# Optimization experiments

Measured on AMD Instinct MI355X. Metric: run time of the kernel, lower is better.

## Reference

```python
import jax, jax.numpy as jnp
import numpy as np

INPUT_DIM = 512
HIDDEN_DIM = 512


def setup_inputs() -> dict:
    key = jax.random.key(0)
    k1, k2 = jax.random.split(key, 2)
    T, B = 2048, 32
    x = jax.random.normal(k1, (T, B, INPUT_DIM), dtype=jnp.float32)
    hidden_state = jnp.zeros((1, B, HIDDEN_DIM), dtype=jnp.float32)
    cell_state = jnp.zeros((1, B, HIDDEN_DIM), dtype=jnp.float32)
    # xavier_uniform for weights, zeros for bias (matches init_weights)
    dim_size = INPUT_DIM + HIDDEN_DIM
    limit = np.sqrt(6.0 / (dim_size + 4 * HIDDEN_DIM)).astype(np.float32)
    weights = jax.random.uniform(k2, (dim_size, 4 * HIDDEN_DIM), dtype=jnp.float32,
                                 minval=-limit, maxval=limit)
    bias = jnp.zeros((4 * HIDDEN_DIM,), dtype=jnp.float32)
    return {"x": x, "hidden_state": hidden_state, "cell_state": cell_state,
            "weights": weights, "bias": bias}


def reference(x, hidden_state, cell_state, weights, bias):
    H = HIDDEN_DIM

    def step(carry, x_t):
        h, c = carry  # [1, B, H] each; x_t: [B, input_dim]
        concat = jnp.concatenate((x_t[None], h), axis=2)  # [1, B, in+H]
        gates = jnp.matmul(concat, weights) + bias        # [1, B, 4H]
        f = jax.nn.sigmoid(gates[:, :, :H])
        i = jax.nn.sigmoid(gates[:, :, H:2 * H])
        g = jnp.tanh(gates[:, :, 2 * H:3 * H])
        o = jax.nn.sigmoid(gates[:, :, 3 * H:])
        c_new = f * c + i * g
        h_new = o * jnp.tanh(c_new)
        return (h_new, c_new), h_new[0]  # emit [B, H]

    (h_f, c_f), outs = jax.lax.scan(step, (hidden_state, cell_state), x)
    return outs, (h_f, c_f)
```

## Files before the change

kernel.cpp:

```cpp
#include <hip/hip_runtime.h>
#include <math.h>

#define T_STEPS 2048
#define BATCH   32
#define IN_DIM  512
#define H_DIM   512
#define G4      2048
#define NWG     16
#define NTHR    512
#define TC      512
#define NCHUNK  4
#define GLS     132

typedef __attribute__((ext_vector_type(8))) short short8;
typedef __attribute__((ext_vector_type(4))) float f32x4;
typedef __attribute__((ext_vector_type(4))) unsigned u32x4;

__device__ inline unsigned short f2bf(float f) {
    unsigned u = __builtin_bit_cast(unsigned, f);
    unsigned r = (u + 0x7FFFu + ((u >> 16) & 1u)) >> 16;
    return (unsigned short)r;
}
__device__ inline unsigned pack2(float a, float b) {
    return (unsigned)f2bf(a) | ((unsigned)f2bf(b) << 16);
}
__device__ inline float fsigm(float x) {
    return __builtin_amdgcn_rcpf(1.f + __expf(-x));
}
__device__ inline float ftanh(float x) {
    return 1.f - 2.f * __builtin_amdgcn_rcpf(__expf(2.f * x) + 1.f);
}
__device__ inline float sigm(float v) { return 1.f / (1.f + expf(-v)); }

__device__ inline void ld4x_ic(const void* p0, const void* p1,
                               const void* p2, const void* p3,
                               u32x4& v0, u32x4& v1, u32x4& v2, u32x4& v3) {
    asm volatile(
        "global_load_dwordx4 %0, %4, off sc1\n\t"
        "global_load_dwordx4 %1, %5, off sc1\n\t"
        "global_load_dwordx4 %2, %6, off sc1\n\t"
        "global_load_dwordx4 %3, %7, off sc1\n\t"
        "s_waitcnt vmcnt(0)"
        : "=&v"(v0), "=&v"(v1), "=&v"(v2), "=&v"(v3)
        : "v"(p0), "v"(p1), "v"(p2), "v"(p3) : "memory");
}

__global__ __launch_bounds__(256) void wt_kernel(const float* __restrict__ W,
                                                 unsigned short* __restrict__ Wt) {
    __shared__ unsigned short tile[32][33];
    const int n0 = blockIdx.x << 5, k0 = blockIdx.y << 5;
    const int tx = threadIdx.x & 31, ty = threadIdx.x >> 5;
    #pragma unroll
    for (int r = 0; r < 32; r += 8)
        tile[ty + r][tx] = f2bf(W[(size_t)(k0 + ty + r) * G4 + n0 + tx]);
    __syncthreads();
    #pragma unroll
    for (int r = 0; r < 32; r += 8)
        Wt[(size_t)(n0 + ty + r) * 1024 + k0 + tx] = tile[tx][ty + r];
}

__global__ void init_h(const float* __restrict__ h0, unsigned short* __restrict__ hb) {
    int i = blockIdx.x * 256 + threadIdx.x;
    hb[i] = f2bf(h0[i]);
}

__global__ __launch_bounds__(256) void xw_mfma(const float* __restrict__ x,
                                               const unsigned short* __restrict__ Wt,
                                               const float* __restrict__ bias,
                                               float* __restrict__ pre) {
    __shared__ unsigned short As[64][40];
    __shared__ unsigned short Bs[64][40];
    const int tid = threadIdx.x;
    const int w = tid >> 6, l = tid & 63;
    const int m0 = blockIdx.y << 6, n0 = blockIdx.x << 6;
    const int srow = tid >> 2, sseg = (tid & 3) << 3;
    const int arow = (w << 4) + (l & 15);
    const int kb = (l >> 4) << 3;
    f32x4 acc[4] = {};

    for (int kc = 0; kc < 16; ++kc) {
        const float* xs = x + (size_t)(m0 + srow) * IN_DIM + kc * 32 + sseg;
        float4 xa = *(const float4*)xs;
        float4 xb2 = *(const float4*)(xs + 4);
        int4 av;
        av.x = pack2(xa.x, xa.y);  av.y = pack2(xa.z, xa.w);
        av.z = pack2(xb2.x, xb2.y); av.w = pack2(xb2.z, xb2.w);
        *(int4*)&As[srow][sseg] = av;
        *(int4*)&Bs[srow][sseg] = *(const int4*)(Wt + (size_t)(n0 + srow) * 1024 + kc * 32 + sseg);
        __syncthreads();
        short8 af = *(const short8*)&As[arow][kb];
        #pragma unroll
        for (int n = 0; n < 4; ++n) {
            short8 bf = *(const short8*)&Bs[(n << 4) + (l & 15)][kb];
            acc[n] = __builtin_amdgcn_mfma_f32_16x16x32_bf16(af, bf, acc[n], 0, 0, 0);
        }
        __syncthreads();
    }
    #pragma unroll
    for (int n = 0; n < 4; ++n) {
        const int col = n0 + (n << 4) + (l & 15);
        const float bb = bias[col];
        #pragma unroll
        for (int ri = 0; ri < 4; ++ri) {
            const int row = m0 + (w << 4) + ((l >> 4) << 2) + ri;
            pre[(size_t)row * G4 + col] = acc[n][ri] + bb;
        }
    }
}

__global__ __launch_bounds__(NTHR, 1) void lstm_scan(
        const unsigned short* __restrict__ Wt,
        const float* __restrict__ pre,
        const float* __restrict__ cin,
        float* __restrict__ cout,
        unsigned short* __restrict__ hbuf,
        float* __restrict__ outs,
        float* __restrict__ hf, float* __restrict__ cf,
        unsigned int* __restrict__ flags,
        int gt0) {
    __shared__ char Hl[32768];

    const int g = blockIdx.x;
    const int tid = threadIdx.x;
    const int w = tid >> 6, l = tid & 63;

    const int gc = ((w >> 1) << 9) + (g << 5) + ((w & 1) << 4) + (l & 15);
    const int ksub = (l >> 4) << 3;
    short8 wfh[16];
    #pragma unroll
    for (int kc = 0; kc < 16; ++kc)
        wfh[kc] = *(const short8*)(Wt + (size_t)gc * 1024 + 512 + kc * 32 + ksub);

    const int b   = tid >> 4;
    const int hcp = (tid & 15) << 1;
    const int col = (g << 5) + hcp;
    float2 cv = *(const float2*)(cin + (b << 9) + col);

    const int arow0 = l & 15, arow1 = (l & 15) + 16;
    const int kbyte = (l >> 4) << 4;
    const int swz0 = (arow0 & 7) << 4, swz1 = (arow1 & 7) << 4;
    const int lcw = (w << 4) + (l & 15);

    {
        const unsigned short* hp0 = hbuf + ((gt0 & 1) << 14) + (w << 9) + (l << 3);
        u32x4 v0, v1, v2, v3;
        ld4x_ic(hp0, hp0 + 4096, hp0 + 8192, hp0 + 12288, v0, v1, v2, v3);
        char* hd = Hl + w * 1024 + ((l << 4) ^ (w << 4));
        *(u32x4*)hd = v0; *(u32x4*)(hd + 8192) = v1;
        *(u32x4*)(hd + 16384) = v2; *(u32x4*)(hd + 24576) = v3;
    }
    __syncthreads();

    const float* pr0 = pre + (size_t)b * G4 + col;
    float2 pf = *(const float2*)pr0;
    float2 pi = *(const float2*)(pr0 + 512);
    float2 pg = *(const float2*)(pr0 + 1024);
    float2 po = *(const float2*)(pr0 + 1536);

    for (int t = 0; t < TC; ++t) {
        const int gt = gt0 + t;

        f32x4 acc0 = {0.f, 0.f, 0.f, 0.f}, acc1 = {0.f, 0.f, 0.f, 0.f};
        #pragma unroll
        for (int kc = 0; kc < 16; ++kc) {
            const int kb2 = kc * 64 + kbyte;
            short8 ha0 = *(const short8*)(Hl + arow0 * 1024 + (kb2 ^ swz0));
            short8 ha1 = *(const short8*)(Hl + arow1 * 1024 + (kb2 ^ swz1));
            acc0 = __builtin_amdgcn_mfma_f32_16x16x32_bf16(ha0, wfh[kc], acc0, 0, 0, 0);
            acc1 = __builtin_amdgcn_mfma_f32_16x16x32_bf16(ha1, wfh[kc], acc1, 0, 0, 0);
        }
        __syncthreads();

        float* Gl = (float*)Hl;
        #pragma unroll
        for (int ri = 0; ri < 4; ++ri) {
            const int br = ((l >> 4) << 2) + ri;
            Gl[br * GLS + lcw] = acc0[ri];
            Gl[(br + 16) * GLS + lcw] = acc1[ri];
        }
        __syncthreads();

        const int tn = (t + 1 < TC) ? t + 1 : t;
        const float* prn = pre + ((size_t)tn * BATCH + b) * G4 + col;
        const float2 npf = *(const float2*)prn;
        const float2 npi = *(const float2*)(prn + 512);
        const float2 npg = *(const float2*)(prn + 1024);
        const float2 npo = *(const float2*)(prn + 1536);

        const float* grow = Gl + b * GLS + hcp;
        const float f0 = fsigm(grow[0]  + pf.x), f1 = fsigm(grow[1]  + pf.y);
        const float i0 = fsigm(grow[32] + pi.x), i1 = fsigm(grow[33] + pi.y);
        const float g0 = ftanh(grow[64] + pg.x), g1 = ftanh(grow[65] + pg.y);
        const float o0 = fsigm(grow[96] + po.x), o1 = fsigm(grow[97] + po.y);
        cv.x = f0 * cv.x + i0 * g0;
        cv.y = f1 * cv.y + i1 * g1;
        const float hn0 = o0 * ftanh(cv.x);
        const float hn1 = o1 * ftanh(cv.y);
        pf = npf; pi = npi; pg = npg; po = npo;

        *(float2*)(outs + ((size_t)gt << 14) + (b << 9) + col) = make_float2(hn0, hn1);
        {
            unsigned* hdst = (unsigned*)hbuf + (((gt + 1) & 1) << 13) + (b << 8) + (col >> 1);
            const unsigned pk = pack2(hn0, hn1);
            asm volatile("global_store_dword %0, %1, off sc1" :: "v"(hdst), "v"(pk) : "memory");
        }
        if (gt == T_STEPS - 1) {
            *(float2*)(hf + (b << 9) + col) = make_float2(hn0, hn1);
            *(float2*)(cf + (b << 9) + col) = make_float2(cv.x, cv.y);
            break;
        }

        asm volatile("s_waitcnt vmcnt(0)" ::: "memory");
        __syncthreads();
        if (tid == 0)
            atomicAdd(flags + (g << 4), 1u);
        if (tid < 16) {
            unsigned* slot = flags + (tid << 4);
            const unsigned tgt = (unsigned)(gt + 1);
            for (;;) {
                unsigned vb;
                asm volatile("global_load_dword %0, %1, off sc1\n\ts_waitcnt vmcnt(0)"
                             : "=v"(vb) : "v"(slot) : "memory");
                if (vb >= tgt) break;
                __builtin_amdgcn_s_sleep(1);
            }
        }
        __syncthreads();

        {
            const unsigned short* hsrc = hbuf + (((gt + 1) & 1) << 14) + (w << 9) + (l << 3);
            u32x4 v0, v1, v2, v3;
            ld4x_ic(hsrc, hsrc + 4096, hsrc + 8192, hsrc + 12288, v0, v1, v2, v3);
            char* hd = Hl + w * 1024 + ((l << 4) ^ (w << 4));
            *(u32x4*)hd = v0; *(u32x4*)(hd + 8192) = v1;
            *(u32x4*)(hd + 16384) = v2; *(u32x4*)(hd + 24576) = v3;
        }
        __syncthreads();
    }

    cout[(b << 9) + col]     = cv.x;
    cout[(b << 9) + col + 1] = cv.y;
}

__global__ __launch_bounds__(256) void lstm_step(const float* __restrict__ x_t,
                                                 const float* __restrict__ h_prev,
                                                 const float* __restrict__ W,
                                                 const float* __restrict__ bias,
                                                 const float* __restrict__ c_in,
                                                 float* __restrict__ c_out,
                                                 float* __restrict__ h_out,
                                                 float* __restrict__ hf,
                                                 float* __restrict__ cf, int last) {
    const int tid = threadIdx.x;
    const int hcc = tid & 7, b = tid >> 3;
    const int col = blockIdx.x * 8 + hcc;
    float a0 = bias[col], a1 = bias[col + 512], a2 = bias[col + 1024], a3 = bias[col + 1536];
    const float* xr = x_t + (size_t)b * IN_DIM;
    const float* hr = h_prev + (size_t)b * H_DIM;
    for (int k = 0; k < IN_DIM; ++k) {
        const float v = xr[k];
        const float* wk = &W[(size_t)k * G4 + col];
        a0 += v * wk[0]; a1 += v * wk[512]; a2 += v * wk[1024]; a3 += v * wk[1536];
    }
    for (int k = 0; k < H_DIM; ++k) {
        const float v = hr[k];
        const float* wk = &W[(size_t)(512 + k) * G4 + col];
        a0 += v * wk[0]; a1 += v * wk[512]; a2 += v * wk[1024]; a3 += v * wk[1536];
    }
    const float cn = sigm(a0) * c_in[(size_t)b * H_DIM + col] + sigm(a1) * tanhf(a2);
    const float hn = sigm(a3) * tanhf(cn);
    c_out[(size_t)b * H_DIM + col] = cn;
    h_out[(size_t)b * H_DIM + col] = hn;
    if (last) { hf[(size_t)b * H_DIM + col] = hn; cf[(size_t)b * H_DIM + col] = cn; }
}

extern "C" void kernel_launch(void* const* d_in, const int* in_sizes, int n_in,
                              void* d_out, int out_size, void* d_ws, size_t ws_size,
                              hipStream_t stream) {
    const float* x    = (const float*)d_in[0];
    const float* h0   = (const float*)d_in[1];
    const float* c0   = (const float*)d_in[2];
    const float* W    = (const float*)d_in[3];
    const float* bias = (const float*)d_in[4];

    float* outs = (float*)d_out;
    float* hf   = outs + (size_t)T_STEPS * BATCH * H_DIM;
    float* cf   = hf + BATCH * H_DIM;

    const size_t OFF_WT = 134217728ull;
    const size_t OFF_HB = OFF_WT + 4194304ull;
    const size_t OFF_C  = OFF_HB + 65536ull;
    const size_t OFF_FL = OFF_C + 65536ull;
    const size_t NEED   = OFF_FL + 4096ull;

    if (ws_size >= NEED) {
        float* pre          = (float*)d_ws;
        unsigned short* Wt  = (unsigned short*)((char*)d_ws + OFF_WT);
        unsigned short* hb  = (unsigned short*)((char*)d_ws + OFF_HB);
        float* c_ws         = (float*)((char*)d_ws + OFF_C);
        unsigned int* flags = (unsigned int*)((char*)d_ws + OFF_FL);

        hipMemsetAsync(flags, 0, 4096, stream);
        wt_kernel<<<dim3(64, 32), 256, 0, stream>>>(W, Wt);
        init_h<<<64, 256, 0, stream>>>(h0, hb);
        for (int k = 0; k < NCHUNK; ++k) {
            xw_mfma<<<dim3(32, TC * BATCH / 64), 256, 0, stream>>>(
                x + (size_t)k * TC * BATCH * IN_DIM, Wt, bias, pre);
            lstm_scan<<<NWG, NTHR, 0, stream>>>(
                Wt, pre, (k == 0) ? c0 : c_ws, c_ws, hb, outs, hf, cf, flags, k * TC);
        }
    } else {
        float* c_ws = (float*)d_ws;
        for (int t = 0; t < T_STEPS; ++t) {
            const float* hp = t ? outs + (size_t)(t - 1) * BATCH * H_DIM : h0;
            const float* ci = t ? c_ws : c0;
            lstm_step<<<64, 256, 0, stream>>>(x + (size_t)t * BATCH * IN_DIM,
                                              hp, W, bias, ci, c_ws,
                                              outs + (size_t)t * BATCH * H_DIM,
                                              hf, cf, (t == T_STEPS - 1) ? 1 : 0);
        }
    }
}
```

Measured before the change: 7.685 ms.

## Give gate scratch its own LDS buffer and prefetch pre-activations across the barrier

Moves the gate accumulator scratch into a separate shared buffer, which removes one __syncthreads per step that guarded reuse of the H tile. The next step's pre-activation loads are now issued with inline asm after the h stores and before the inter-block barrier, and a partial vmcnt wait lets them stay in flight during the spin-wait. Gate values are read from LDS as float2 and the sleep in the flag polling loop is removed. The manual waitcnt accounting depends on exact instruction ordering. Removing the sleep makes polling more aggressive, which may add memory traffic.

```diff
diff --git a/kernel.cpp b/kernel.cpp
--- a/kernel.cpp
+++ b/kernel.cpp
@@ -14,6 +14,7 @@
 
 typedef __attribute__((ext_vector_type(8))) short short8;
 typedef __attribute__((ext_vector_type(4))) float f32x4;
+typedef __attribute__((ext_vector_type(2))) float f32x2;
 typedef __attribute__((ext_vector_type(4))) unsigned u32x4;
 
 __device__ inline unsigned short f2bf(float f) {
@@ -119,6 +120,7 @@
         unsigned int* __restrict__ flags,
         int gt0) {
     __shared__ char Hl[32768];
+    __shared__ float Gl[32 * GLS];
 
     const int g = blockIdx.x;
     const int tid = threadIdx.x;
@@ -151,11 +153,14 @@
     }
     __syncthreads();
 
-    const float* pr0 = pre + (size_t)b * G4 + col;
-    float2 pf = *(const float2*)pr0;
-    float2 pi = *(const float2*)(pr0 + 512);
-    float2 pg = *(const float2*)(pr0 + 1024);
-    float2 po = *(const float2*)(pr0 + 1536);
+    f32x2 pf, pi, pg, po;
+    {
+        const float* pr0 = pre + (size_t)b * G4 + col;
+        asm volatile("global_load_dwordx2 %0, %1, off" : "=v"(pf) : "v"(pr0) : "memory");
+        asm volatile("global_load_dwordx2 %0, %1, off" : "=v"(pi) : "v"(pr0 + 512) : "memory");
+        asm volatile("global_load_dwordx2 %0, %1, off" : "=v"(pg) : "v"(pr0 + 1024) : "memory");
+        asm volatile("global_load_dwordx2 %0, %1, off" : "=v"(po) : "v"(pr0 + 1536) : "memory");
+    }
 
     for (int t = 0; t < TC; ++t) {
         const int gt = gt0 + t;
@@ -169,9 +174,7 @@
             acc0 = __builtin_amdgcn_mfma_f32_16x16x32_bf16(ha0, wfh[kc], acc0, 0, 0, 0);
             acc1 = __builtin_amdgcn_mfma_f32_16x16x32_bf16(ha1, wfh[kc], acc1, 0, 0, 0);
         }
-        __syncthreads();
-
-        float* Gl = (float*)Hl;
+
         #pragma unroll
         for (int ri = 0; ri < 4; ++ri) {
             const int br = ((l >> 4) << 2) + ri;
@@ -180,26 +183,27 @@
         }
         __syncthreads();
 
-        const int tn = (t + 1 < TC) ? t + 1 : t;
-        const float* prn = pre + ((size_t)tn * BATCH + b) * G4 + col;
-        const float2 npf = *(const float2*)prn;
-        const float2 npi = *(const float2*)(prn + 512);
-        const float2 npg = *(const float2*)(prn + 1024);
-        const float2 npo = *(const float2*)(prn + 1536);
+        asm volatile("s_waitcnt vmcnt(0)" ::: "memory");
+        __builtin_amdgcn_sched_barrier(0);
 
         const float* grow = Gl + b * GLS + hcp;
-        const float f0 = fsigm(grow[0]  + pf.x), f1 = fsigm(grow[1]  + pf.y);
-        const float i0 = fsigm(grow[32] + pi.x), i1 = fsigm(grow[33] + pi.y);
-        const float g0 = ftanh(grow[64] + pg.x), g1 = ftanh(grow[65] + pg.y);
-        const float o0 = fsigm(grow[96] + po.x), o1 = fsigm(grow[97] + po.y);
+        const float2 g_f = *(const float2*)(grow);
+        const float2 g_i = *(const float2*)(grow + 32);
+        const float2 g_g = *(const float2*)(grow + 64);
+        const float2 g_o = *(const float2*)(grow + 96);
+        const float f0 = fsigm(g_f.x + pf.x), f1 = fsigm(g_f.y + pf.y);
+        const float i0 = fsigm(g_i.x + pi.x), i1 = fsigm(g_i.y + pi.y);
+        const float g0 = ftanh(g_g.x + pg.x), g1 = ftanh(g_g.y + pg.y);
+        const float o0 = fsigm(g_o.x + po.x), o1 = fsigm(g_o.y + po.y);
         cv.x = f0 * cv.x + i0 * g0;
         cv.y = f1 * cv.y + i1 * g1;
         const float hn0 = o0 * ftanh(cv.x);
         const float hn1 = o1 * ftanh(cv.y);
-        pf = npf; pi = npi; pg = npg; po = npo;
-
-        *(float2*)(outs + ((size_t)gt << 14) + (b << 9) + col) = make_float2(hn0, hn1);
+
         {
+            float* optr = outs + ((size_t)gt << 14) + (b << 9) + col;
+            f32x2 ov; ov.x = hn0; ov.y = hn1;
+            asm volatile("global_store_dwordx2 %0, %1, off" :: "v"(optr), "v"(ov) : "memory");
             unsigned* hdst = (unsigned*)hbuf + (((gt + 1) & 1) << 13) + (b << 8) + (col >> 1);
             const unsigned pk = pack2(hn0, hn1);
             asm volatile("global_store_dword %0, %1, off sc1" :: "v"(hdst), "v"(pk) : "memory");
@@ -210,7 +214,16 @@
             break;
         }
 
-        asm volatile("s_waitcnt vmcnt(0)" ::: "memory");
+        {
+            const int tn = (t + 1 < TC) ? t + 1 : t;
+            const float* prn = pre + ((size_t)tn * BATCH + b) * G4 + col;
+            asm volatile("global_load_dwordx2 %0, %1, off" : "=v"(pf) : "v"(prn) : "memory");
+            asm volatile("global_load_dwordx2 %0, %1, off" : "=v"(pi) : "v"(prn + 512) : "memory");
+            asm volatile("global_load_dwordx2 %0, %1, off" : "=v"(pg) : "v"(prn + 1024) : "memory");
+            asm volatile("global_load_dwordx2 %0, %1, off" : "=v"(po) : "v"(prn + 1536) : "memory");
+        }
+        asm volatile("s_waitcnt vmcnt(4)" ::: "memory");
+
         __syncthreads();
         if (tid == 0)
             atomicAdd(flags + (g << 4), 1u);
@@ -222,7 +235,6 @@
                 asm volatile("global_load_dword %0, %1, off sc1\n\ts_waitcnt vmcnt(0)"
                              : "=v"(vb) : "v"(slot) : "memory");
                 if (vb >= tgt) break;
-                __builtin_amdgcn_s_sleep(1);
             }
         }
         __syncthreads();
```

Result: faster. 7.483 ms (-2.6%).
